# Kernel optimization log

Measured on AMD Instinct MI355X. Metric: run time of the kernel, lower is better.

## Reference

```python
import jax, jax.numpy as jnp
import numpy as np

B, C, T, H, W = 2, 512, 8, 16, 16
NUM_HEADS = 8
HEAD_DIM = C // NUM_HEADS


def setup_inputs() -> dict:
    key = jax.random.key(0)
    ks = jax.random.split(key, 6)
    x = jax.random.normal(ks[0], (B, C, T, H, W), dtype=jnp.float32)
    # LayerNorm params
    ln_w = jnp.ones((C,), dtype=jnp.float32)
    ln_b = jnp.zeros((C,), dtype=jnp.float32)
    # 1x1x1 Conv3d == per-token linear; weight stored [out, in]
    w_qkv = jax.random.normal(ks[1], (3 * C, C), dtype=jnp.float32) * (1.0 / np.sqrt(C))
    b_qkv = jnp.zeros((3 * C,), dtype=jnp.float32)
    w_proj = jax.random.normal(ks[2], (C, C), dtype=jnp.float32) * (1.0 / np.sqrt(C))
    b_proj = jnp.zeros((C,), dtype=jnp.float32)
    return {"x": x, "ln_w": ln_w, "ln_b": ln_b, "w_qkv": w_qkv,
            "b_qkv": b_qkv, "w_proj": w_proj, "b_proj": b_proj}


def reference(x, ln_w, ln_b, w_qkv, b_qkv, w_proj, b_proj):
    Bx, Cx, Tx, Hx, Wx = x.shape
    N = Tx * Hx * Wx
    scale = HEAD_DIM ** -0.5

    # [B,C,T,H,W] -> [B,N,C]
    x_flat = jnp.transpose(x, (0, 2, 3, 4, 1)).reshape(Bx, N, Cx)

    # LayerNorm over channels
    mu = jnp.mean(x_flat, axis=-1, keepdims=True)
    var = jnp.var(x_flat, axis=-1, keepdims=True)
    x_flat = (x_flat - mu) * jax.lax.rsqrt(var + 1e-5) * ln_w + ln_b

    # QKV (1x1x1 conv == linear). Output channel layout: [3, heads, head_dim]
    qkv = jnp.einsum('bnc,oc->bno', x_flat, w_qkv) + b_qkv  # [B,N,3C]
    qkv = qkv.reshape(Bx, N, 3, NUM_HEADS, HEAD_DIM)
    qkv = jnp.transpose(qkv, (2, 0, 3, 1, 4))  # [3,B,heads,N,head_dim]
    q, k, v = qkv[0], qkv[1], qkv[2]

    attn = jnp.einsum('bhnd,bhmd->bhnm', q, k) * scale
    attn = jax.nn.softmax(attn, axis=-1)
    x_attn = jnp.einsum('bhnm,bhmd->bhnd', attn, v)  # [B,heads,N,head_dim]
    x_attn = jnp.transpose(x_attn, (0, 2, 1, 3)).reshape(Bx, N, Cx)

    # proj (1x1x1 conv == linear)
    x_attn = jnp.einsum('bnc,oc->bno', x_attn, w_proj) + b_proj

    # NOTE: residual is on the *normalized* x_flat (as in the original module)
    x_out = x_flat + x_attn
    x_out = x_out.reshape(Bx, Tx, Hx, Wx, Cx)
    return jnp.transpose(x_out, (0, 4, 1, 2, 3))  # [B,C,T,H,W]
```

## Files before the change

kernel.cpp:

```cpp
#include <hip/hip_runtime.h>
#include <hip/hip_bf16.h>

#define BB 2
#define CC 512
#define NN 2048
#define NHEADS 8
#define HDIM 64
#define NSPLIT 2
#define KVQ 1024

typedef __attribute__((ext_vector_type(8))) __bf16 bf16x8;
typedef __attribute__((ext_vector_type(4))) __bf16 bf16x4;
typedef __attribute__((ext_vector_type(4))) float f32x4;

typedef const __attribute__((address_space(1))) unsigned int guint;
typedef __attribute__((address_space(3))) unsigned int suint;

#define QSCALE 0.18033688f
#define MFIX 32.0f

__global__ __launch_bounds__(256) void ln_cvt_kernel(
    const float* __restrict__ x, const float* __restrict__ lnw,
    const float* __restrict__ lnb, const float* __restrict__ wqkv,
    const float* __restrict__ wproj, float* __restrict__ mu,
    float* __restrict__ rstd, __bf16* __restrict__ xln_t,
    __bf16* __restrict__ wqkv_bf, __bf16* __restrict__ wproj_bf) {
  __shared__ float Xs[512][20];
  __shared__ float rs[16][17];
  __shared__ float rq[16][17];
  __shared__ float mloc[16];
  __shared__ float rloc[16];
  int tid = threadIdx.x;
  if (blockIdx.x >= 256) {
    int i = (blockIdx.x - 256) * 256 + tid;
    const int NQ = 3 * CC * CC / 4;
    if (i < NQ) {
      float4 v = *(const float4*)&wqkv[(size_t)i * 4];
      bf16x4 pk = {(__bf16)v.x, (__bf16)v.y, (__bf16)v.z, (__bf16)v.w};
      *(bf16x4*)&wqkv_bf[(size_t)i * 4] = pk;
    } else {
      int j = i - NQ;
      float4 v = *(const float4*)&wproj[(size_t)j * 4];
      bf16x4 pk = {(__bf16)v.x, (__bf16)v.y, (__bf16)v.z, (__bf16)v.w};
      *(bf16x4*)&wproj_bf[(size_t)j * 4] = pk;
    }
    return;
  }
  int bid = blockIdx.x & 127;
  int b = blockIdx.x >> 7;
  int n_tile = 2 * (((bid >> 4) << 3) + (bid & 7)) + ((bid >> 3) & 1);
  int n0 = n_tile * 16;
#pragma unroll
  for (int l = 0; l < 8; ++l) {
    int e = tid + 256 * l;
    int row = e >> 2, quad = e & 3;
    float4 v = *(const float4*)&x[((size_t)b * CC + row) * NN + n0 + quad * 4];
    *(float4*)&Xs[row][quad * 4] = v;
  }
  __syncthreads();
  {
    int tk = tid & 15, part = tid >> 4;
    float s = 0.f, ss = 0.f;
    int c0 = part * 32;
#pragma unroll 8
    for (int j = 0; j < 32; ++j) {
      float v = Xs[c0 + j][tk];
      s += v;
      ss += v * v;
    }
    rs[part][tk] = s;
    rq[part][tk] = ss;
  }
  __syncthreads();
  if (tid < 16) {
    float S = 0.f, SS = 0.f;
#pragma unroll
    for (int p = 0; p < 16; ++p) {
      S += rs[p][tid];
      SS += rq[p][tid];
    }
    float m = S * (1.0f / CC);
    float var = SS * (1.0f / CC) - m * m;
    float rv = rsqrtf(var + 1e-5f);
    mloc[tid] = m;
    rloc[tid] = rv;
    int tok = b * NN + n0 + tid;
    mu[tok] = m;
    rstd[tok] = rv;
  }
  __syncthreads();
  {
    int tk = tid >> 4;
    int cseg = (tid & 15) * 32;
    float mun = mloc[tk], rsn = rloc[tk];
    __bf16 outv[32];
#pragma unroll
    for (int j = 0; j < 32; ++j) {
      int c = cseg + j;
      outv[j] = (__bf16)((Xs[c][tk] - mun) * rsn * lnw[c] + lnb[c]);
    }
    __bf16* dst = &xln_t[((size_t)b * NN + n0 + tk) * CC + cseg];
#pragma unroll
    for (int q = 0; q < 4; ++q) *(bf16x8*)&dst[q * 8] = *(bf16x8*)&outv[q * 8];
  }
}

__global__ __launch_bounds__(256, 3) void qkv_mfma_kernel(
    const __bf16* __restrict__ xln_t, const __bf16* __restrict__ wbf,
    const float* __restrict__ bias, __bf16* __restrict__ qt,
    __bf16* __restrict__ kt, __bf16* __restrict__ vbf) {
  __shared__ __align__(16) __bf16 As[2][64][64];
  __shared__ __align__(16) __bf16 Bs[2][128][64];
  int n0 = blockIdx.x * 128;
  bool swap = blockIdx.y < 16;
  int m0 = swap ? blockIdx.y * 64 : 1024 + ((int)blockIdx.y - 16) * 64;
  int b = blockIdx.z;
  int tid = threadIdx.x;
  int wid = tid >> 6, lane = tid & 63;
  int g = lane >> 4, c = lane & 15;
  int wr = wid >> 1, wc = wid & 1;
  const __bf16* xln = xln_t + (size_t)b * NN * CC;
  int l7 = lane & 7, l3 = lane >> 3;
  int xr = (l7 ^ l3) * 8;
  auto STAGE = [&](int buf, int k0) {
#pragma unroll
    for (int j = 0; j < 2; ++j) {
      int r = wid * 16 + 8 * j + l3;
      __builtin_amdgcn_global_load_lds(
          (guint*)(wbf + (size_t)(m0 + r) * CC + k0 + xr),
          (suint*)&As[buf][wid * 16 + 8 * j][0], 16, 0, 0);
    }
#pragma unroll
    for (int j = 0; j < 4; ++j) {
      int r = wid * 32 + 8 * j + l3;
      __builtin_amdgcn_global_load_lds(
          (guint*)(xln + (size_t)(n0 + r) * CC + k0 + xr),
          (suint*)&Bs[buf][wid * 32 + 8 * j][0], 16, 0, 0);
    }
  };
  STAGE(0, 0);
  f32x4 acc[2][4] = {};
  int cxor = c & 7;
  for (int ks = 0; ks < 8; ++ks) {
    int cur = ks & 1;
    if (ks < 7) {
      STAGE(cur ^ 1, (ks + 1) * 64);
      asm volatile("s_waitcnt vmcnt(6)" ::: "memory");
    } else {
      asm volatile("s_waitcnt vmcnt(0)" ::: "memory");
    }
    __builtin_amdgcn_sched_barrier(0);
    __builtin_amdgcn_s_barrier();
    __builtin_amdgcn_s_setprio(1);
#pragma unroll
    for (int hh = 0; hh < 2; ++hh) {
      int ch = ((hh * 4 + g) ^ cxor) * 8;
      bf16x8 af[2], bfr[4];
#pragma unroll
      for (int mi = 0; mi < 2; ++mi)
        af[mi] = *(const bf16x8*)&As[cur][wr * 32 + mi * 16 + c][ch];
#pragma unroll
      for (int nj = 0; nj < 4; ++nj)
        bfr[nj] = *(const bf16x8*)&Bs[cur][wc * 64 + nj * 16 + c][ch];
      if (swap) {
#pragma unroll
        for (int mi = 0; mi < 2; ++mi)
#pragma unroll
          for (int nj = 0; nj < 4; ++nj)
            acc[mi][nj] = __builtin_amdgcn_mfma_f32_16x16x32_bf16(
                bfr[nj], af[mi], acc[mi][nj], 0, 0, 0);
      } else {
#pragma unroll
        for (int mi = 0; mi < 2; ++mi)
#pragma unroll
          for (int nj = 0; nj < 4; ++nj)
            acc[mi][nj] = __builtin_amdgcn_mfma_f32_16x16x32_bf16(
                af[mi], bfr[nj], acc[mi][nj], 0, 0, 0);
      }
    }
    __builtin_amdgcn_s_setprio(0);
    __builtin_amdgcn_s_barrier();
  }
  if (swap) {
    int obase = m0 + wr * 32;
    int sec = obase >> 9;
    int osec = obase & 511;
    int head = osec >> 6;
    int dbase = osec & 63;
    __bf16* dst = (sec == 0 ? qt : kt) + (size_t)(b * NHEADS + head) * NN * HDIM;
    float scl = (sec == 0) ? QSCALE : 1.0f;
#pragma unroll
    for (int mi = 0; mi < 2; ++mi) {
      float bo = bias[obase + mi * 16 + c];
      int d = dbase + mi * 16 + c;
#pragma unroll
      for (int nj = 0; nj < 4; ++nj)
#pragma unroll
        for (int r = 0; r < 4; ++r) {
          int n = n0 + wc * 64 + nj * 16 + 4 * g + r;
          dst[(size_t)n * HDIM + d] = (__bf16)((acc[mi][nj][r] + bo) * scl);
        }
    }
  } else {
#pragma unroll
    for (int mi = 0; mi < 2; ++mi)
#pragma unroll
      for (int r = 0; r < 4; ++r) {
        int o = m0 + wr * 32 + mi * 16 + 4 * g + r;
        int ch = o - 1024;
        float bo = bias[o];
#pragma unroll
        for (int nj = 0; nj < 4; ++nj) {
          int n = n0 + wc * 64 + nj * 16 + c;
          vbf[((size_t)b * CC + ch) * NN + n] = (__bf16)(acc[mi][nj][r] + bo);
        }
      }
  }
}

__global__ __launch_bounds__(256, 3) void attn_mfma_kernel(
    const __bf16* __restrict__ qt, const __bf16* __restrict__ ktg,
    const __bf16* __restrict__ vbf, __bf16* __restrict__ opart,
    float* __restrict__ lbuf) {
  __shared__ __align__(16) __bf16 Kb[2][64][64];
  __shared__ __align__(16) __bf16 Vb[2][64][64];
  int tid = threadIdx.x;
  int wid = tid >> 6, lane = tid & 63;
  int g = lane >> 4, c = lane & 15;
  int n0 = blockIdx.x * 128;
  int h = blockIdx.y;
  int b = blockIdx.z >> 1, split = blockIdx.z & 1;
  int bh = b * NHEADS + h;
  const __bf16* qbase = qt + ((size_t)bh * NN + n0) * HDIM;
  const __bf16* kbase = ktg + ((size_t)bh * NN + split * KVQ) * HDIM;
  const __bf16* vbase = vbf + ((size_t)b * CC + h * HDIM) * NN + split * KVQ;

  int l7 = lane & 7, l3 = lane >> 3;
  int xr = (l7 ^ l3) * 8;
  auto STAGE = [&](int buf, int mt) {
#pragma unroll
    for (int j = 0; j < 2; ++j) {
      int r = wid * 16 + 8 * j + l3;
      int gr = (r & 0x20) | (((r >> 2) & 3) << 3) | (((r >> 4) & 1) << 2) | (r & 3);
      const __bf16* ksrc = kbase + (size_t)(mt + gr) * HDIM + xr;
      __builtin_amdgcn_global_load_lds((guint*)ksrc,
                                       (suint*)&Kb[buf][wid * 16 + 8 * j][0],
                                       16, 0, 0);
      const __bf16* vsrc = vbase + (size_t)r * NN + mt + xr;
      __builtin_amdgcn_global_load_lds((guint*)vsrc,
                                       (suint*)&Vb[buf][wid * 16 + 8 * j][0],
                                       16, 0, 0);
    }
  };

  STAGE(0, 0);
  bf16x8 aq[2][2];
#pragma unroll
  for (int qg = 0; qg < 2; ++qg) {
    const __bf16* qp = qbase + (size_t)(wid * 32 + qg * 16 + c) * HDIM;
    aq[qg][0] = *(const bf16x8*)(qp + g * 8);
    aq[qg][1] = *(const bf16x8*)(qp + 32 + g * 8);
  }
  f32x4 O[2][4] = {};
  f32x4 Ol[2] = {};
  int cxor = (c & 7);
  const f32x4 cinit = {-MFIX, -MFIX, -MFIX, -MFIX};
  const bf16x8 vones = {(__bf16)1.f, (__bf16)1.f, (__bf16)1.f, (__bf16)1.f,
                        (__bf16)1.f, (__bf16)1.f, (__bf16)1.f, (__bf16)1.f};

  for (int t = 0; t < KVQ / 64; ++t) {
    int cur = t & 1;
    if (t + 1 < KVQ / 64) {
      STAGE(cur ^ 1, (t + 1) * 64);
      asm volatile("s_waitcnt vmcnt(4)" ::: "memory");
    } else {
      asm volatile("s_waitcnt vmcnt(0)" ::: "memory");
    }
    __builtin_amdgcn_sched_barrier(0);
    __builtin_amdgcn_s_barrier();
    f32x4 st[2][4];
    __builtin_amdgcn_s_setprio(1);
#pragma unroll
    for (int t4 = 0; t4 < 4; ++t4) {
      bf16x8 bk0 = *(const bf16x8*)&Kb[cur][t4 * 16 + c][(g ^ cxor) * 8];
      bf16x8 bk1 = *(const bf16x8*)&Kb[cur][t4 * 16 + c][((4 + g) ^ cxor) * 8];
#pragma unroll
      for (int qg = 0; qg < 2; ++qg) {
        f32x4 acc = __builtin_amdgcn_mfma_f32_16x16x32_bf16(bk0, aq[qg][0],
                                                            cinit, 0, 0, 0);
        acc = __builtin_amdgcn_mfma_f32_16x16x32_bf16(bk1, aq[qg][1], acc, 0, 0, 0);
        st[qg][t4] = acc;
      }
    }
    __builtin_amdgcn_s_setprio(0);
    bf16x8 pa[2][2];
#pragma unroll
    for (int qg = 0; qg < 2; ++qg) {
#pragma unroll
      for (int t4 = 0; t4 < 4; ++t4) {
        float p0 = exp2f(st[qg][t4][0]);
        float p1 = exp2f(st[qg][t4][1]);
        float p2 = exp2f(st[qg][t4][2]);
        float p3 = exp2f(st[qg][t4][3]);
        bf16x8* pp = &pa[qg][t4 >> 1];
        int o4 = (t4 & 1) * 4;
        (*pp)[o4 + 0] = (__bf16)p0;
        (*pp)[o4 + 1] = (__bf16)p1;
        (*pp)[o4 + 2] = (__bf16)p2;
        (*pp)[o4 + 3] = (__bf16)p3;
      }
    }
    __builtin_amdgcn_s_setprio(1);
#pragma unroll
    for (int dt = 0; dt < 4; ++dt) {
      bf16x8 bv0 = *(const bf16x8*)&Vb[cur][dt * 16 + c][(g ^ cxor) * 8];
      bf16x8 bv1 = *(const bf16x8*)&Vb[cur][dt * 16 + c][((4 + g) ^ cxor) * 8];
#pragma unroll
      for (int qg = 0; qg < 2; ++qg) {
        O[qg][dt] = __builtin_amdgcn_mfma_f32_16x16x32_bf16(bv0, pa[qg][0],
                                                            O[qg][dt], 0, 0, 0);
        O[qg][dt] = __builtin_amdgcn_mfma_f32_16x16x32_bf16(bv1, pa[qg][1],
                                                            O[qg][dt], 0, 0, 0);
      }
    }
#pragma unroll
    for (int qg = 0; qg < 2; ++qg) {
      Ol[qg] = __builtin_amdgcn_mfma_f32_16x16x32_bf16(vones, pa[qg][0],
                                                       Ol[qg], 0, 0, 0);
      Ol[qg] = __builtin_amdgcn_mfma_f32_16x16x32_bf16(vones, pa[qg][1],
                                                       Ol[qg], 0, 0, 0);
    }
    __builtin_amdgcn_s_setprio(0);
    __builtin_amdgcn_s_barrier();
  }
#pragma unroll
  for (int qg = 0; qg < 2; ++qg) {
    size_t prow = ((size_t)(split * BB + b) * NHEADS + h) * NN +
                  (n0 + wid * 32 + qg * 16 + c);
#pragma unroll
    for (int dt = 0; dt < 4; ++dt) {
      bf16x4 pk = {(__bf16)O[qg][dt][0], (__bf16)O[qg][dt][1],
                   (__bf16)O[qg][dt][2], (__bf16)O[qg][dt][3]};
      *(bf16x4*)&opart[prow * HDIM + dt * 16 + 4 * g] = pk;
    }
    if (lane < 16) lbuf[prow] = Ol[qg][0];
  }
}

__global__ __launch_bounds__(256, 4) void proj_fused_kernel(
    const __bf16* __restrict__ opart, const float* __restrict__ lbuf,
    const __bf16* __restrict__ wbf, const float* __restrict__ bias,
    const float* __restrict__ x, const float* __restrict__ mu,
    const float* __restrict__ rstd, const float* __restrict__ lnw,
    const float* __restrict__ lnb, float* __restrict__ out) {
  __shared__ __align__(16) __bf16 As[2][64][64];
  __shared__ __align__(16) __bf16 Bs[2][64][64];
  int n0 = blockIdx.x * 64;
  int m0 = blockIdx.y * 64;
  int b = blockIdx.z;
  int tid = threadIdx.x;
  int wid = tid >> 6, lane = tid & 63;
  int g = lane >> 4, c = lane & 15;
  int wr = wid >> 1, wc = wid & 1;
  int l7 = lane & 7, l3 = lane >> 3;
  int xr = (l7 ^ l3) * 8;
  auto STAGE_A = [&](int buf, int k0) {
#pragma unroll
    for (int j = 0; j < 2; ++j) {
      int r = wid * 16 + 8 * j + l3;
      __builtin_amdgcn_global_load_lds(
          (guint*)(wbf + (size_t)(m0 + r) * CC + k0 + xr),
          (suint*)&As[buf][wid * 16 + 8 * j][0], 16, 0, 0);
    }
  };
  int rB = tid >> 2, qB = tid & 3;
  bf16x8 b0[2], b1[2];
  float l0, l1;
  auto LOAD_B = [&](int h) {
    size_t p0 = ((size_t)(0 * BB + b) * NHEADS + h) * NN + n0 + rB;
    size_t p1 = ((size_t)(1 * BB + b) * NHEADS + h) * NN + n0 + rB;
    b0[0] = *(const bf16x8*)&opart[p0 * HDIM + qB * 16];
    b0[1] = *(const bf16x8*)&opart[p0 * HDIM + qB * 16 + 8];
    b1[0] = *(const bf16x8*)&opart[p1 * HDIM + qB * 16];
    b1[1] = *(const bf16x8*)&opart[p1 * HDIM + qB * 16 + 8];
    l0 = lbuf[p0];
    l1 = lbuf[p1];
  };
  auto WRITE_B = [&](int buf) {
    float linv = 1.0f / (l0 + l1);
#pragma unroll
    for (int ch = 0; ch < 2; ++ch) {
      __bf16 ov[8];
#pragma unroll
      for (int j = 0; j < 8; ++j)
        ov[j] = (__bf16)(((float)b0[ch][j] + (float)b1[ch][j]) * linv);
      int chunk = (qB * 2 + ch) ^ (rB & 7);
      *(bf16x8*)&Bs[buf][rB][chunk * 8] = *(bf16x8*)&ov;
    }
  };

  LOAD_B(0);
  STAGE_A(0, 0);
  asm volatile("s_waitcnt vmcnt(0)" ::: "memory");
  __builtin_amdgcn_sched_barrier(0);
  WRITE_B(0);
  __syncthreads();

  f32x4 acc[2][2] = {};
  int cxor = c & 7;
  for (int ks = 0; ks < 8; ++ks) {
    int cur = ks & 1;
    if (ks < 7) {
      STAGE_A(cur ^ 1, (ks + 1) * 64);
      LOAD_B(ks + 1);
    }
    __builtin_amdgcn_s_setprio(1);
#pragma unroll
    for (int hh = 0; hh < 2; ++hh) {
      int ch = ((hh * 4 + g) ^ cxor) * 8;
      bf16x8 af[2], bfr[2];
#pragma unroll
      for (int mi = 0; mi < 2; ++mi)
        af[mi] = *(const bf16x8*)&As[cur][wr * 32 + mi * 16 + c][ch];
#pragma unroll
      for (int nj = 0; nj < 2; ++nj)
        bfr[nj] = *(const bf16x8*)&Bs[cur][wc * 32 + nj * 16 + c][ch];
#pragma unroll
      for (int mi = 0; mi < 2; ++mi)
#pragma unroll
        for (int nj = 0; nj < 2; ++nj)
          acc[mi][nj] = __builtin_amdgcn_mfma_f32_16x16x32_bf16(
              af[mi], bfr[nj], acc[mi][nj], 0, 0, 0);
    }
    __builtin_amdgcn_s_setprio(0);
    __builtin_amdgcn_s_barrier();
    if (ks < 7) {
      asm volatile("s_waitcnt vmcnt(0)" ::: "memory");
      __builtin_amdgcn_sched_barrier(0);
      WRITE_B(cur ^ 1);
      asm volatile("s_waitcnt lgkmcnt(0)" ::: "memory");
    }
    __builtin_amdgcn_s_barrier();
  }
#pragma unroll
  for (int mi = 0; mi < 2; ++mi)
#pragma unroll
    for (int r = 0; r < 4; ++r) {
      int o = m0 + wr * 32 + mi * 16 + 4 * g + r;
      float bo = bias[o], gw = lnw[o], gb = lnb[o];
#pragma unroll
      for (int nj = 0; nj < 2; ++nj) {
        int n = n0 + wc * 32 + nj * 16 + c;
        int tok = b * NN + n;
        float xv = x[((size_t)b * CC + o) * NN + n];
        float xlnv = (xv - mu[tok]) * rstd[tok] * gw + gb;
        out[((size_t)b * CC + o) * NN + n] = acc[mi][nj][r] + bo + xlnv;
      }
    }
}

extern "C" void kernel_launch(void* const* d_in, const int* in_sizes, int n_in,
                              void* d_out, int out_size, void* d_ws, size_t ws_size,
                              hipStream_t stream) {
  const float* x = (const float*)d_in[0];
  const float* lnw = (const float*)d_in[1];
  const float* lnb = (const float*)d_in[2];
  const float* wqkv = (const float*)d_in[3];
  const float* bqkv = (const float*)d_in[4];
  const float* wproj = (const float*)d_in[5];
  const float* bproj = (const float*)d_in[6];
  float* out = (float*)d_out;
  (void)in_sizes; (void)n_in; (void)out_size; (void)ws_size;

  char* wsb = (char*)d_ws;
  float* mu = (float*)wsb;
  float* rstd = mu + 4096;
  const size_t HSZ = (size_t)BB * NHEADS * NN * HDIM;
  __bf16* qt = (__bf16*)(wsb + 32768);
  __bf16* kt = qt + HSZ;
  __bf16* vbf = kt + HSZ;
  __bf16* xln_t = vbf + HSZ;
  __bf16* opart = xln_t + HSZ;
  float* lbuf = (float*)(opart + (size_t)NSPLIT * HSZ);
  __bf16* wqkv_bf = (__bf16*)((char*)lbuf + 524288);
  __bf16* wproj_bf = wqkv_bf + (size_t)3 * CC * CC;

  hipLaunchKernelGGL(ln_cvt_kernel, dim3(1280), dim3(256), 0, stream,
                     x, lnw, lnb, wqkv, wproj, mu, rstd, xln_t, wqkv_bf,
                     wproj_bf);
  hipLaunchKernelGGL(qkv_mfma_kernel, dim3(16, 24, 2), dim3(256), 0, stream,
                     xln_t, wqkv_bf, bqkv, qt, kt, vbf);
  hipLaunchKernelGGL(attn_mfma_kernel, dim3(16, 8, BB * NSPLIT), dim3(256), 0,
                     stream, qt, kt, vbf, opart, lbuf);
  hipLaunchKernelGGL(proj_fused_kernel, dim3(32, 8, 2), dim3(256), 0, stream,
                     opart, lbuf, wproj_bf, bproj, x, mu, rstd, lnw, lnb, out);
}
```

Measured before the change: 67.76 us.

## Widen attention query tiles, split KV four ways, add separate combine kernel

The attention kernel now handles 256 queries per block (64 per wave) and splits the KV sequence four ways, so each staged K/V tile is reused across twice as many queries. The split partials are reduced by a new combine kernel that writes a token-major bf16 attention output. The projection GEMM then loads both operands directly into LDS with async global-to-LDS copies, no longer merging partials inside its pipeline. This adds an extra kernel launch and a full round trip of the partials through memory, and raises register pressure (occupancy hint lowered to 2) in exchange for fewer redundant K/V loads.

```diff
diff --git a/kernel.cpp b/kernel.cpp
--- a/kernel.cpp
+++ b/kernel.cpp
@@ -6,8 +6,8 @@
 #define NN 2048
 #define NHEADS 8
 #define HDIM 64
-#define NSPLIT 2
-#define KVQ 1024
+#define NSPLIT 4
+#define KVQ 512
 
 typedef __attribute__((ext_vector_type(8))) __bf16 bf16x8;
 typedef __attribute__((ext_vector_type(4))) __bf16 bf16x4;
@@ -218,7 +218,7 @@
   }
 }
 
-__global__ __launch_bounds__(256, 3) void attn_mfma_kernel(
+__global__ __launch_bounds__(256, 2) void attn_mfma_kernel(
     const __bf16* __restrict__ qt, const __bf16* __restrict__ ktg,
     const __bf16* __restrict__ vbf, __bf16* __restrict__ opart,
     float* __restrict__ lbuf) {
@@ -227,9 +227,9 @@
   int tid = threadIdx.x;
   int wid = tid >> 6, lane = tid & 63;
   int g = lane >> 4, c = lane & 15;
-  int n0 = blockIdx.x * 128;
+  int n0 = blockIdx.x * 256;
   int h = blockIdx.y;
-  int b = blockIdx.z >> 1, split = blockIdx.z & 1;
+  int b = blockIdx.z >> 2, split = blockIdx.z & 3;
   int bh = b * NHEADS + h;
   const __bf16* qbase = qt + ((size_t)bh * NN + n0) * HDIM;
   const __bf16* kbase = ktg + ((size_t)bh * NN + split * KVQ) * HDIM;
@@ -254,15 +254,15 @@
   };
 
   STAGE(0, 0);
-  bf16x8 aq[2][2];
-#pragma unroll
-  for (int qg = 0; qg < 2; ++qg) {
-    const __bf16* qp = qbase + (size_t)(wid * 32 + qg * 16 + c) * HDIM;
+  bf16x8 aq[4][2];
+#pragma unroll
+  for (int qg = 0; qg < 4; ++qg) {
+    const __bf16* qp = qbase + (size_t)(wid * 64 + qg * 16 + c) * HDIM;
     aq[qg][0] = *(const bf16x8*)(qp + g * 8);
     aq[qg][1] = *(const bf16x8*)(qp + 32 + g * 8);
   }
-  f32x4 O[2][4] = {};
-  f32x4 Ol[2] = {};
+  f32x4 O[4][4] = {};
+  f32x4 Ol[4] = {};
   int cxor = (c & 7);
   const f32x4 cinit = {-MFIX, -MFIX, -MFIX, -MFIX};
   const bf16x8 vones = {(__bf16)1.f, (__bf16)1.f, (__bf16)1.f, (__bf16)1.f,
@@ -278,30 +278,33 @@
     }
     __builtin_amdgcn_sched_barrier(0);
     __builtin_amdgcn_s_barrier();
-    f32x4 st[2][4];
+    bf16x8 bk0[4], bk1[4];
     __builtin_amdgcn_s_setprio(1);
 #pragma unroll
     for (int t4 = 0; t4 < 4; ++t4) {
-      bf16x8 bk0 = *(const bf16x8*)&Kb[cur][t4 * 16 + c][(g ^ cxor) * 8];
-      bf16x8 bk1 = *(const bf16x8*)&Kb[cur][t4 * 16 + c][((4 + g) ^ cxor) * 8];
-#pragma unroll
-      for (int qg = 0; qg < 2; ++qg) {
-        f32x4 acc = __builtin_amdgcn_mfma_f32_16x16x32_bf16(bk0, aq[qg][0],
-                                                            cinit, 0, 0, 0);
-        acc = __builtin_amdgcn_mfma_f32_16x16x32_bf16(bk1, aq[qg][1], acc, 0, 0, 0);
-        st[qg][t4] = acc;
-      }
+      bk0[t4] = *(const bf16x8*)&Kb[cur][t4 * 16 + c][(g ^ cxor) * 8];
+      bk1[t4] = *(const bf16x8*)&Kb[cur][t4 * 16 + c][((4 + g) ^ cxor) * 8];
     }
     __builtin_amdgcn_s_setprio(0);
-    bf16x8 pa[2][2];
-#pragma unroll
-    for (int qg = 0; qg < 2; ++qg) {
+    bf16x8 pa[4][2];
+#pragma unroll
+    for (int qg = 0; qg < 4; ++qg) {
+      f32x4 st[4];
+      __builtin_amdgcn_s_setprio(1);
 #pragma unroll
       for (int t4 = 0; t4 < 4; ++t4) {
-        float p0 = exp2f(st[qg][t4][0]);
-        float p1 = exp2f(st[qg][t4][1]);
-        float p2 = exp2f(st[qg][t4][2]);
-        float p3 = exp2f(st[qg][t4][3]);
+        f32x4 a = __builtin_amdgcn_mfma_f32_16x16x32_bf16(bk0[t4], aq[qg][0],
+                                                          cinit, 0, 0, 0);
+        st[t4] = __builtin_amdgcn_mfma_f32_16x16x32_bf16(bk1[t4], aq[qg][1],
+                                                         a, 0, 0, 0);
+      }
+      __builtin_amdgcn_s_setprio(0);
+#pragma unroll
+      for (int t4 = 0; t4 < 4; ++t4) {
+        float p0 = exp2f(st[t4][0]);
+        float p1 = exp2f(st[t4][1]);
+        float p2 = exp2f(st[t4][2]);
+        float p3 = exp2f(st[t4][3]);
         bf16x8* pp = &pa[qg][t4 >> 1];
         int o4 = (t4 & 1) * 4;
         (*pp)[o4 + 0] = (__bf16)p0;
@@ -316,7 +319,7 @@
       bf16x8 bv0 = *(const bf16x8*)&Vb[cur][dt * 16 + c][(g ^ cxor) * 8];
       bf16x8 bv1 = *(const bf16x8*)&Vb[cur][dt * 16 + c][((4 + g) ^ cxor) * 8];
 #pragma unroll
-      for (int qg = 0; qg < 2; ++qg) {
+      for (int qg = 0; qg < 4; ++qg) {
         O[qg][dt] = __builtin_amdgcn_mfma_f32_16x16x32_bf16(bv0, pa[qg][0],
                                                             O[qg][dt], 0, 0, 0);
         O[qg][dt] = __builtin_amdgcn_mfma_f32_16x16x32_bf16(bv1, pa[qg][1],
@@ -324,7 +327,7 @@
       }
     }
 #pragma unroll
-    for (int qg = 0; qg < 2; ++qg) {
+    for (int qg = 0; qg < 4; ++qg) {
       Ol[qg] = __builtin_amdgcn_mfma_f32_16x16x32_bf16(vones, pa[qg][0],
                                                        Ol[qg], 0, 0, 0);
       Ol[qg] = __builtin_amdgcn_mfma_f32_16x16x32_bf16(vones, pa[qg][1],
@@ -334,9 +337,9 @@
     __builtin_amdgcn_s_barrier();
   }
 #pragma unroll
-  for (int qg = 0; qg < 2; ++qg) {
+  for (int qg = 0; qg < 4; ++qg) {
     size_t prow = ((size_t)(split * BB + b) * NHEADS + h) * NN +
-                  (n0 + wid * 32 + qg * 16 + c);
+                  (n0 + wid * 64 + qg * 16 + c);
 #pragma unroll
     for (int dt = 0; dt < 4; ++dt) {
       bf16x4 pk = {(__bf16)O[qg][dt][0], (__bf16)O[qg][dt][1],
@@ -347,12 +350,38 @@
   }
 }
 
-__global__ __launch_bounds__(256, 4) void proj_fused_kernel(
+__global__ __launch_bounds__(256) void attn_combine_kernel(
     const __bf16* __restrict__ opart, const float* __restrict__ lbuf,
-    const __bf16* __restrict__ wbf, const float* __restrict__ bias,
-    const float* __restrict__ x, const float* __restrict__ mu,
-    const float* __restrict__ rstd, const float* __restrict__ lnw,
-    const float* __restrict__ lnb, float* __restrict__ out) {
+    __bf16* __restrict__ xa_t) {
+  int t = threadIdx.x;
+  int row_local = t >> 4;
+  int dq = (t & 15) * 4;
+  int R = blockIdx.x * 16 + row_local;
+  int n = R & (NN - 1);
+  int bh = R >> 11;
+  int b = bh >> 3, h = bh & 7;
+  float lsum = 0.f;
+  float acc[4] = {0.f, 0.f, 0.f, 0.f};
+#pragma unroll
+  for (int s = 0; s < NSPLIT; ++s) {
+    size_t p = ((size_t)(s * BB + b) * NHEADS + h) * NN + n;
+    lsum += lbuf[p];
+    bf16x4 ov = *(const bf16x4*)&opart[p * HDIM + dq];
+#pragma unroll
+    for (int j = 0; j < 4; ++j) acc[j] += (float)ov[j];
+  }
+  float linv = 1.0f / lsum;
+  bf16x4 pk = {(__bf16)(acc[0] * linv), (__bf16)(acc[1] * linv),
+               (__bf16)(acc[2] * linv), (__bf16)(acc[3] * linv)};
+  *(bf16x4*)&xa_t[((size_t)b * NN + n) * CC + h * HDIM + dq] = pk;
+}
+
+__global__ __launch_bounds__(256, 4) void proj_mfma_kernel(
+    const __bf16* __restrict__ xa_t, const __bf16* __restrict__ wbf,
+    const float* __restrict__ bias, const float* __restrict__ x,
+    const float* __restrict__ mu, const float* __restrict__ rstd,
+    const float* __restrict__ lnw, const float* __restrict__ lnb,
+    float* __restrict__ out) {
   __shared__ __align__(16) __bf16 As[2][64][64];
   __shared__ __align__(16) __bf16 Bs[2][64][64];
   int n0 = blockIdx.x * 64;
@@ -362,58 +391,34 @@
   int wid = tid >> 6, lane = tid & 63;
   int g = lane >> 4, c = lane & 15;
   int wr = wid >> 1, wc = wid & 1;
+  const __bf16* xab = xa_t + (size_t)b * NN * CC;
   int l7 = lane & 7, l3 = lane >> 3;
   int xr = (l7 ^ l3) * 8;
-  auto STAGE_A = [&](int buf, int k0) {
+  auto STAGE = [&](int buf, int k0) {
 #pragma unroll
     for (int j = 0; j < 2; ++j) {
       int r = wid * 16 + 8 * j + l3;
       __builtin_amdgcn_global_load_lds(
           (guint*)(wbf + (size_t)(m0 + r) * CC + k0 + xr),
           (suint*)&As[buf][wid * 16 + 8 * j][0], 16, 0, 0);
+      __builtin_amdgcn_global_load_lds(
+          (guint*)(xab + (size_t)(n0 + r) * CC + k0 + xr),
+          (suint*)&Bs[buf][wid * 16 + 8 * j][0], 16, 0, 0);
     }
   };
-  int rB = tid >> 2, qB = tid & 3;
-  bf16x8 b0[2], b1[2];
-  float l0, l1;
-  auto LOAD_B = [&](int h) {
-    size_t p0 = ((size_t)(0 * BB + b) * NHEADS + h) * NN + n0 + rB;
-    size_t p1 = ((size_t)(1 * BB + b) * NHEADS + h) * NN + n0 + rB;
-    b0[0] = *(const bf16x8*)&opart[p0 * HDIM + qB * 16];
-    b0[1] = *(const bf16x8*)&opart[p0 * HDIM + qB * 16 + 8];
-    b1[0] = *(const bf16x8*)&opart[p1 * HDIM + qB * 16];
-    b1[1] = *(const bf16x8*)&opart[p1 * HDIM + qB * 16 + 8];
-    l0 = lbuf[p0];
-    l1 = lbuf[p1];
-  };
-  auto WRITE_B = [&](int buf) {
-    float linv = 1.0f / (l0 + l1);
-#pragma unroll
-    for (int ch = 0; ch < 2; ++ch) {
-      __bf16 ov[8];
-#pragma unroll
-      for (int j = 0; j < 8; ++j)
-        ov[j] = (__bf16)(((float)b0[ch][j] + (float)b1[ch][j]) * linv);
-      int chunk = (qB * 2 + ch) ^ (rB & 7);
-      *(bf16x8*)&Bs[buf][rB][chunk * 8] = *(bf16x8*)&ov;
-    }
-  };
-
-  LOAD_B(0);
-  STAGE_A(0, 0);
-  asm volatile("s_waitcnt vmcnt(0)" ::: "memory");
-  __builtin_amdgcn_sched_barrier(0);
-  WRITE_B(0);
-  __syncthreads();
-
+  STAGE(0, 0);
   f32x4 acc[2][2] = {};
   int cxor = c & 7;
   for (int ks = 0; ks < 8; ++ks) {
     int cur = ks & 1;
     if (ks < 7) {
-      STAGE_A(cur ^ 1, (ks + 1) * 64);
-      LOAD_B(ks + 1);
-    }
+      STAGE(cur ^ 1, (ks + 1) * 64);
+      asm volatile("s_waitcnt vmcnt(4)" ::: "memory");
+    } else {
+      asm volatile("s_waitcnt vmcnt(0)" ::: "memory");
+    }
+    __builtin_amdgcn_sched_barrier(0);
+    __builtin_amdgcn_s_barrier();
     __builtin_amdgcn_s_setprio(1);
 #pragma unroll
     for (int hh = 0; hh < 2; ++hh) {
@@ -433,13 +438,6 @@
               af[mi], bfr[nj], acc[mi][nj], 0, 0, 0);
     }
     __builtin_amdgcn_s_setprio(0);
-    __builtin_amdgcn_s_barrier();
-    if (ks < 7) {
-      asm volatile("s_waitcnt vmcnt(0)" ::: "memory");
-      __builtin_amdgcn_sched_barrier(0);
-      WRITE_B(cur ^ 1);
-      asm volatile("s_waitcnt lgkmcnt(0)" ::: "memory");
-    }
     __builtin_amdgcn_s_barrier();
   }
 #pragma unroll
@@ -480,18 +478,22 @@
   __bf16* kt = qt + HSZ;
   __bf16* vbf = kt + HSZ;
   __bf16* xln_t = vbf + HSZ;
-  __bf16* opart = xln_t + HSZ;
-  float* lbuf = (float*)(opart + (size_t)NSPLIT * HSZ);
+  __bf16* opart = xln_t;
+  float* lbuf = (float*)(wsb + 32768 + 3 * HSZ * sizeof(__bf16) +
+                         (size_t)NSPLIT * HSZ * sizeof(__bf16));
   __bf16* wqkv_bf = (__bf16*)((char*)lbuf + 524288);
   __bf16* wproj_bf = wqkv_bf + (size_t)3 * CC * CC;
+  __bf16* xa_t = qt;
 
   hipLaunchKernelGGL(ln_cvt_kernel, dim3(1280), dim3(256), 0, stream,
                      x, lnw, lnb, wqkv, wproj, mu, rstd, xln_t, wqkv_bf,
                      wproj_bf);
   hipLaunchKernelGGL(qkv_mfma_kernel, dim3(16, 24, 2), dim3(256), 0, stream,
                      xln_t, wqkv_bf, bqkv, qt, kt, vbf);
-  hipLaunchKernelGGL(attn_mfma_kernel, dim3(16, 8, BB * NSPLIT), dim3(256), 0,
+  hipLaunchKernelGGL(attn_mfma_kernel, dim3(8, 8, BB * NSPLIT), dim3(256), 0,
                      stream, qt, kt, vbf, opart, lbuf);
-  hipLaunchKernelGGL(proj_fused_kernel, dim3(32, 8, 2), dim3(256), 0, stream,
-                     opart, lbuf, wproj_bf, bproj, x, mu, rstd, lnw, lnb, out);
-}
+  hipLaunchKernelGGL(attn_combine_kernel, dim3(2048), dim3(256), 0, stream,
+                     opart, lbuf, xa_t);
+  hipLaunchKernelGGL(proj_mfma_kernel, dim3(32, 8, 2), dim3(256), 0, stream,
+                     xa_t, wproj_bf, bproj, x, mu, rstd, lnw, lnb, out);
+}
```

Result: slower. 69.88 us (+3.1%).
